# Optimization experiments

Measured on AMD Instinct MI355X. Metric: run time of the kernel, lower is better.

Reference implementation:

```python
import jax, jax.numpy as jnp
import numpy as np
from functools import partial

SAMPLE_RATE = 48000
BITRATE = 128000
M = 1024            # AAC_FRAME_LENGTH (hop, MDCT bins)
N = 2048            # AAC_WINDOW_LENGTH
TARGET_BITS = BITRATE * M / SAMPLE_RATE   # bits per frame (all channels)
MAX_GAIN = 120.0
EPS = 1e-9


def _window():
    # sine window satisfies Princen-Bradley: w[n]^2 + w[n+M]^2 = 1
    n = jnp.arange(N, dtype=jnp.float32)
    return jnp.sin(jnp.pi / N * (n + 0.5))


def _cosmat():
    # MDCT basis  C[n,k] = cos(pi/M (n + 0.5 + M/2)(k + 0.5)),  shape (N, M)
    n = jnp.arange(N, dtype=jnp.float32)[:, None]
    k = jnp.arange(M, dtype=jnp.float32)[None, :]
    return jnp.cos(jnp.pi / M * (n + 0.5 + M / 2) * (k + 0.5))


def _frame_bits(ax75, gain):
    """Estimated coded bits per frame under hard AAC power-law quantization.
    ax75: |coeff|^{3/4}, shape (B,F,C,M); gain: (B,F)."""
    inv = jnp.exp2(-0.75 * gain / 4.0)[:, :, None, None]
    qmag = jnp.round(ax75 * inv)
    # sign-magnitude style cost: nonzero -> floor(log2|q|)+2 bits, zero -> 1 bit
    bits = jnp.where(qmag > 0.0,
                     jnp.floor(jnp.log2(jnp.maximum(qmag, 1.0))) + 2.0,
                     1.0)
    return jnp.sum(bits, axis=(2, 3))  # (B,F)


def _find_global_gain(coeffs_bfcm):
    """Integer binary search for smallest gain with bits <= TARGET_BITS. (no grad)"""
    ax75 = jnp.abs(jax.lax.stop_gradient(coeffs_bfcm)) ** 0.75
    B, F = ax75.shape[0], ax75.shape[1]
    lo = jnp.zeros((B, F), jnp.float32)
    hi = jnp.full((B, F), MAX_GAIN, jnp.float32)

    def body(_, carry):
        lo, hi = carry
        mid = jnp.floor((lo + hi) / 2.0)
        too_big = _frame_bits(ax75, mid) > TARGET_BITS
        lo = jnp.where(too_big, mid + 1.0, lo)
        hi = jnp.where(too_big, hi, mid)
        return lo, hi

    _, hi = jax.lax.fori_loop(0, 8, body, (lo, hi))  # 8 iters covers [0,120]
    return hi  # (B,F)


def reference(audio):
    B, C, T = audio.shape
    w = _window()
    Cm = _cosmat()

    # --- frame_audio: left-pad M, right-pad to full frames ---
    F = -(-(T + M) // M)
    pad_right = F * M + M - (T + M)
    x = jnp.pad(audio, ((0, 0), (0, 0), (M, pad_right)))
    idx = jnp.arange(F)[:, None] * M + jnp.arange(N)[None, :]      # (F,N)
    frames = x[:, :, idx]                                          # (B,C,F,N)

    # --- analysis window + MDCT ---
    windowed = frames * w
    coeffs = jnp.einsum('bcfn,nk->bcfk', windowed, Cm)             # (B,C,F,M)
    coeffs_bfcm = jnp.transpose(coeffs, (0, 2, 1, 3))              # (B,F,C,M)

    # --- iterative global-gain search (hard quant, no grad) ---
    gains = _find_global_gain(coeffs_bfcm)                         # (B,F)

    # --- quantize (STE) / dequantize: q = round((|x| 2^{-g/4})^{3/4}) ---
    scale = jnp.exp2(gains / 4.0)[:, :, None, None]
    sgn = jnp.sign(coeffs_bfcm)
    q_soft = sgn * (jnp.abs(coeffs_bfcm) / scale + EPS) ** 0.75
    q = q_soft + jax.lax.stop_gradient(jnp.round(q_soft) - q_soft)
    dq = jnp.sign(q) * jnp.abs(q) ** (4.0 / 3.0) * scale           # (B,F,C,M)

    # --- IMDCT + synthesis window ---
    dq_bcfm = jnp.transpose(dq, (0, 2, 1, 3))                      # (B,C,F,M)
    td = (2.0 / M) * jnp.einsum('bcfk,nk->bcfn', dq_bcfm, Cm)      # (B,C,F,N)
    rew = td * w

    # --- overlap-add (hop M) ---
    out = jnp.zeros((B, C, (F + 1) * M), audio.dtype)
    out = out.at[:, :, :F * M].add(rew[:, :, :, :M].reshape(B, C, F * M))
    out = out.at[:, :, M:].add(rew[:, :, :, M:].reshape(B, C, F * M))
    return out[:, :, M:M + T]


def setup_inputs() -> dict:
    key = jax.random.key(0)
    audio = 0.5 * jax.random.normal(key, (8, 2, 1440000), dtype=jnp.float32)
    return {"audio": audio}
```

## Files before the change

kernel.cpp:

```cpp
#include <hip/hip_runtime.h>
#include <math.h>

#define B_ 8
#define C_ 2
#define T_ 1440000
#define F_ 1408
#define R_ 22528
#define TARGET_HI 2731

#define OFF_CFH 0ull
#define OFF_CFL (4ull << 20)
#define OFF_CIH (8ull << 20)
#define OFF_WF  (12ull << 20)
#define OFF_CF  (13ull << 20)
#define OFF_DQ  (OFF_CF + (size_t)R_ * 1024 * 4)

typedef _Float16 f16x8 __attribute__((ext_vector_type(8)));
typedef _Float16 f16x4 __attribute__((ext_vector_type(4)));
typedef float f32x16 __attribute__((ext_vector_type(16)));

__device__ inline f32x16 mfma16(f16x8 a, f16x8 b, f32x16 c) {
  return __builtin_amdgcn_mfma_f32_32x32x16_f16(a, b, c, 0, 0, 0);
}

__device__ inline void gld_lds16(const void* g, void* l) {
  __builtin_amdgcn_global_load_lds(
      (const __attribute__((address_space(1))) void*)g,
      (__attribute__((address_space(3))) void*)l, 16, 0, 0);
}

__global__ __launch_bounds__(256) void init_tables(char* wsb) {
  _Float16* cfh = (_Float16*)(wsb + OFF_CFH);
  _Float16* cfl = (_Float16*)(wsb + OFF_CFL);
  _Float16* cih = (_Float16*)(wsb + OFF_CIH);
  float*    wf  = (float*)(wsb + OFF_WF);
  int idx = blockIdx.x * 256 + threadIdx.x;
  if (idx < 2097152) {
    int n = idx >> 10, k = idx & 1023;
    const float c0 = (float)(M_PI / 1024.0);
    float a  = (float)n + 0.5f + 512.0f;
    float t1 = c0 * a;
    float ph = t1 * ((float)k + 0.5f);
    float cm = (float)cos((double)ph);
    _Float16 h = (_Float16)cm;
    _Float16 l = (_Float16)(cm - (float)h);
    cfh[(size_t)k * 2048 + n] = h;
    cfl[(size_t)k * 2048 + n] = l;
    cih[(size_t)n * 1024 + k] = h;
  } else if (idx < 2097152 + 2048) {
    int n = idx - 2097152;
    const float c1 = (float)(M_PI / 2048.0);
    float ph = c1 * ((float)n + 0.5f);
    wf[n] = (float)sin((double)ph);
  }
}

__global__ __launch_bounds__(256) void fwd_mfma(const float* __restrict__ audio,
                                                const char* __restrict__ wsb,
                                                float* __restrict__ coeffs) {
  __shared__ _Float16 Ah[128][40];
  __shared__ _Float16 Al[128][40];
  __shared__ _Float16 Bh[128][40];
  __shared__ _Float16 Bl[128][40];
  const _Float16* cfh = (const _Float16*)(wsb + OFF_CFH);
  const _Float16* cfl = (const _Float16*)(wsb + OFF_CFL);
  const float*    wf  = (const float*)(wsb + OFF_WF);

  int tid = threadIdx.x;
  int lane = tid & 63, wid = tid >> 6;
  int l31 = lane & 31, lHalf = lane >> 5;
  int waveM = wid >> 1, waveN = wid & 1;
  int rowTile = blockIdx.x * 128, colTile = blockIdx.y * 128;

  int sRow = tid >> 1;
  int sSeg = (tid & 1) << 4;
  int r = rowTile + sRow, bc = r / F_, f = r - bc * F_;
  const float* __restrict__ aud = audio + (size_t)bc * T_;
  int tBase = (f << 10) - 1024 + sSeg;
  const _Float16* bhp = cfh + (size_t)(colTile + sRow) * 2048 + sSeg;
  const _Float16* blp = cfl + (size_t)(colTile + sRow) * 2048 + sSeg;

  f32x16 acc[2][2];
#pragma unroll
  for (int i = 0; i < 2; i++)
#pragma unroll
    for (int j = 0; j < 2; j++)
#pragma unroll
      for (int e = 0; e < 16; e++) acc[i][j][e] = 0.f;

  for (int kt = 0; kt < 2048; kt += 32) {
    float av[16];
    int t0 = tBase + kt;
    if (t0 >= 0 && t0 + 16 <= T_) {
#pragma unroll
      for (int q = 0; q < 4; q++) {
        float4 x = *(const float4*)(aud + t0 + q * 4);
        av[q * 4 + 0] = x.x; av[q * 4 + 1] = x.y;
        av[q * 4 + 2] = x.z; av[q * 4 + 3] = x.w;
      }
    } else {
#pragma unroll
      for (int i = 0; i < 16; i++) {
        int t = t0 + i;
        av[i] = (t >= 0 && t < T_) ? aud[t] : 0.f;
      }
    }
    f16x8 vh[2], vl[2];
#pragma unroll
    for (int i = 0; i < 16; i++) {
      float v = av[i] * wf[kt + sSeg + i];
      _Float16 h = (_Float16)v;
      vh[i >> 3][i & 7] = h;
      vl[i >> 3][i & 7] = (_Float16)(v - (float)h);
    }
    float4 tb0 = *(const float4*)(bhp + kt);
    float4 tb1 = *(const float4*)(bhp + kt + 8);
    float4 tl0 = *(const float4*)(blp + kt);
    float4 tl1 = *(const float4*)(blp + kt + 8);

    __syncthreads();
    *(f16x8*)&Ah[sRow][sSeg]     = vh[0];
    *(f16x8*)&Ah[sRow][sSeg + 8] = vh[1];
    *(f16x8*)&Al[sRow][sSeg]     = vl[0];
    *(f16x8*)&Al[sRow][sSeg + 8] = vl[1];
    *(float4*)&Bh[sRow][sSeg]     = tb0;
    *(float4*)&Bh[sRow][sSeg + 8] = tb1;
    *(float4*)&Bl[sRow][sSeg]     = tl0;
    *(float4*)&Bl[sRow][sSeg + 8] = tl1;
    __syncthreads();

#pragma unroll
    for (int kc = 0; kc < 2; kc++) {
      int ko = kc * 16 + lHalf * 8;
      f16x8 a_h[2], a_l[2], b_h[2], b_l[2];
#pragma unroll
      for (int mi = 0; mi < 2; mi++) {
        a_h[mi] = *(const f16x8*)&Ah[waveM * 64 + mi * 32 + l31][ko];
        a_l[mi] = *(const f16x8*)&Al[waveM * 64 + mi * 32 + l31][ko];
      }
#pragma unroll
      for (int ni = 0; ni < 2; ni++) {
        b_h[ni] = *(const f16x8*)&Bh[waveN * 64 + ni * 32 + l31][ko];
        b_l[ni] = *(const f16x8*)&Bl[waveN * 64 + ni * 32 + l31][ko];
      }
#pragma unroll
      for (int mi = 0; mi < 2; mi++)
#pragma unroll
        for (int ni = 0; ni < 2; ni++) {
          acc[mi][ni] = mfma16(a_h[mi], b_h[ni], acc[mi][ni]);
          acc[mi][ni] = mfma16(a_h[mi], b_l[ni], acc[mi][ni]);
          acc[mi][ni] = mfma16(a_l[mi], b_h[ni], acc[mi][ni]);
        }
    }
  }

#pragma unroll
  for (int mi = 0; mi < 2; mi++)
#pragma unroll
    for (int ni = 0; ni < 2; ni++) {
      int col = colTile + waveN * 64 + ni * 32 + l31;
#pragma unroll
      for (int reg = 0; reg < 16; reg++) {
        int rowIn = (reg & 3) + 8 * (reg >> 2) + 4 * lHalf;
        int rr = rowTile + waveM * 64 + mi * 32 + rowIn;
        coeffs[(size_t)rr * 1024 + col] = acc[mi][ni][reg];
      }
    }
}

__global__ __launch_bounds__(256) void quantize(const float* __restrict__ cf,
                                                _Float16* __restrict__ dqh) {
  int wid = threadIdx.x >> 6, lane = threadIdx.x & 63;
  int bf = blockIdx.x * 4 + wid;
  int b = bf / F_, f = bf - b * F_;
  size_t base0 = ((size_t)(b * C_ + 0) * F_ + f) * 1024;
  size_t base1 = ((size_t)(b * C_ + 1) * F_ + f) * 1024;

  float x[32], ax75[32];
#pragma unroll
  for (int c = 0; c < 2; c++) {
    size_t bb = c ? base1 : base0;
#pragma unroll
    for (int j = 0; j < 4; j++) {
      float4 v = *(const float4*)(cf + bb + j * 256 + lane * 4);
      int o = c * 16 + j * 4;
      x[o + 0] = v.x; x[o + 1] = v.y; x[o + 2] = v.z; x[o + 3] = v.w;
    }
  }
#pragma unroll
  for (int u = 0; u < 32; u++) {
    float ax = fabsf(x[u]);
    float s  = sqrtf(ax);
    ax75[u]  = s * sqrtf(s);
  }

  int lo = 0, hi = 120;
#pragma unroll
  for (int it = 0; it < 8; it++) {
    int mid = (lo + hi) >> 1;
    float inv = exp2f(-0.1875f * (float)mid);
    int s = 0;
#pragma unroll
    for (int u = 0; u < 32; u++) {
      float qm = rintf(ax75[u] * inv);
      int iq = (int)qm;
      s += (iq > 0) ? (33 - __clz(iq)) : 1;
    }
#pragma unroll
    for (int off = 1; off < 64; off <<= 1) s += __shfl_xor(s, off, 64);
    if (s >= TARGET_HI) lo = mid + 1; else hi = mid;
  }

  float scale = exp2f(0.25f * (float)hi);
  float rs    = exp2f(-0.25f * (float)hi);
#pragma unroll
  for (int c = 0; c < 2; c++) {
    size_t bb = c ? base1 : base0;
#pragma unroll
    for (int j = 0; j < 4; j++) {
      f16x4 o4;
#pragma unroll
      for (int e = 0; e < 4; e++) {
        int u = c * 16 + j * 4 + e;
        float ax  = fabsf(x[u]);
        float t   = ax * rs + 1e-9f;
        float s1  = sqrtf(t);
        float qs  = s1 * sqrtf(s1);
        float q   = rintf(qs);
        float q43 = q * exp2f(__log2f(q) * (1.0f / 3.0f));
        o4[e] = (_Float16)copysignf(q43 * scale, x[u]);
      }
      *(f16x4*)(dqh + bb + j * 256 + lane * 4) = o4;
    }
  }
}

__global__ __launch_bounds__(256) void inv_gemm(const char* __restrict__ wsb,
                                                _Float16* __restrict__ tdh) {
  __shared__ __align__(16) _Float16 Ad[2][128][32];
  __shared__ __align__(16) _Float16 Bd[2][256][32];
  const _Float16* dqh = (const _Float16*)(wsb + OFF_DQ);
  const _Float16* cih = (const _Float16*)(wsb + OFF_CIH);
  const float*    wf  = (const float*)(wsb + OFF_WF);

  int tid = threadIdx.x;
  int lane = tid & 63, wid = tid >> 6;
  int l31 = lane & 31, lHalf = lane >> 5;
  int waveM = wid >> 1, waveN = wid & 1;
  int rowTile = blockIdx.x * 128, colTile = blockIdx.y * 256;

  int srcRow = lane >> 2;
  int swz = ((lane & 3) ^ ((lane >> 3) & 3)) << 3;
  const _Float16* aS = dqh + (size_t)(rowTile + wid * 32 + srcRow) * 1024 + swz;
  const _Float16* bS = cih + (size_t)(colTile + wid * 64 + srcRow) * 1024 + swz;

  auto stage = [&](int kt, int buf) {
    gld_lds16(aS + kt,             &Ad[buf][wid * 32][0]);
    gld_lds16(aS + kt + 16 * 1024, &Ad[buf][wid * 32 + 16][0]);
#pragma unroll
    for (int j = 0; j < 4; j++)
      gld_lds16(bS + kt + (size_t)j * 16 * 1024, &Bd[buf][wid * 64 + j * 16][0]);
  };

  f32x16 acc[2][4];
#pragma unroll
  for (int i = 0; i < 2; i++)
#pragma unroll
    for (int j = 0; j < 4; j++)
#pragma unroll
      for (int e = 0; e < 16; e++) acc[i][j][e] = 0.f;

  stage(0, 0);
  asm volatile("s_waitcnt vmcnt(0)" ::: "memory");
  __syncthreads();

  int cur = 0;
  for (int kt = 0; kt < 1024; kt += 32) {
    if (kt + 32 < 1024) stage(kt + 32, cur ^ 1);
#pragma unroll
    for (int kc = 0; kc < 2; kc++) {
      int slot = ((kc * 2 + lHalf) ^ ((l31 >> 1) & 3)) << 4;
      const char* ar = (const char*)&Ad[cur][waveM * 64 + l31][0];
      const char* br = (const char*)&Bd[cur][waveN * 128 + l31][0];
      f16x8 a0 = *(const f16x8*)(ar + slot);
      f16x8 a1 = *(const f16x8*)(ar + 32 * 64 + slot);
      f16x8 b0 = *(const f16x8*)(br + slot);
      f16x8 b1 = *(const f16x8*)(br + 32 * 64 + slot);
      f16x8 b2 = *(const f16x8*)(br + 64 * 64 + slot);
      f16x8 b3 = *(const f16x8*)(br + 96 * 64 + slot);
      acc[0][0] = mfma16(a0, b0, acc[0][0]);
      acc[0][1] = mfma16(a0, b1, acc[0][1]);
      acc[0][2] = mfma16(a0, b2, acc[0][2]);
      acc[0][3] = mfma16(a0, b3, acc[0][3]);
      acc[1][0] = mfma16(a1, b0, acc[1][0]);
      acc[1][1] = mfma16(a1, b1, acc[1][1]);
      acc[1][2] = mfma16(a1, b2, acc[1][2]);
      acc[1][3] = mfma16(a1, b3, acc[1][3]);
    }
    asm volatile("s_waitcnt vmcnt(0)" ::: "memory");
    __syncthreads();
    cur ^= 1;
  }

  const float sc = 2.0f / 1024.0f;
#pragma unroll
  for (int mi = 0; mi < 2; mi++)
#pragma unroll
    for (int ni = 0; ni < 4; ni++) {
      int n = colTile + waveN * 128 + ni * 32 + l31;
      float wv = wf[n] * sc;
#pragma unroll
      for (int reg = 0; reg < 16; reg++) {
        int rowIn = (reg & 3) + 8 * (reg >> 2) + 4 * lHalf;
        int rr = rowTile + waveM * 64 + mi * 32 + rowIn;
        tdh[(size_t)rr * 2048 + n] = (_Float16)(acc[mi][ni][reg] * wv);
      }
    }
}

__global__ __launch_bounds__(256) void ola(const char* __restrict__ wsb,
                                           float* __restrict__ out) {
  const _Float16* tdh = (const _Float16*)(wsb + OFF_CF);
  int idx = blockIdx.x * 256 + threadIdx.x;
  size_t base = (size_t)idx * 8;
  int bc = (int)(base / T_);
  int t  = (int)(base - (size_t)bc * T_);
  int g = t >> 10, o = t & 1023;
  size_t r0 = (size_t)bc * F_ + g;
  f16x8 hi = *(const f16x8*)(tdh + (r0 + 1) * 2048 + o);
  f16x8 lo = *(const f16x8*)(tdh + r0 * 2048 + 1024 + o);
  float4 v0, v1;
  v0.x = (float)hi[0] + (float)lo[0];
  v0.y = (float)hi[1] + (float)lo[1];
  v0.z = (float)hi[2] + (float)lo[2];
  v0.w = (float)hi[3] + (float)lo[3];
  v1.x = (float)hi[4] + (float)lo[4];
  v1.y = (float)hi[5] + (float)lo[5];
  v1.z = (float)hi[6] + (float)lo[6];
  v1.w = (float)hi[7] + (float)lo[7];
  *(float4*)(out + base)     = v0;
  *(float4*)(out + base + 4) = v1;
}

extern "C" void kernel_launch(void* const* d_in, const int* in_sizes, int n_in,
                              void* d_out, int out_size, void* d_ws, size_t ws_size,
                              hipStream_t stream) {
  const float* audio = (const float*)d_in[0];
  float* out = (float*)d_out;
  char* wsb  = (char*)d_ws;
  float*    cf  = (float*)(wsb + OFF_CF);
  _Float16* dqh = (_Float16*)(wsb + OFF_DQ);
  _Float16* tdh = (_Float16*)(wsb + OFF_CF);

  init_tables<<<(2097152 + 2048 + 255) / 256, 256, 0, stream>>>(wsb);
  fwd_mfma<<<dim3(R_ / 128, 1024 / 128), 256, 0, stream>>>(audio, wsb, cf);
  quantize<<<(B_ * F_) / 4, 256, 0, stream>>>(cf, dqh);
  inv_gemm<<<dim3(R_ / 128, 2048 / 256), 256, 0, stream>>>(wsb, tdh);
  ola<<<(B_ * C_ * T_) / (256 * 8), 256, 0, stream>>>(wsb, out);
}
```

Before: 798.1 us.

## Exploit IMDCT output symmetry to halve inverse GEMM columns

Because the IMDCT output has even/odd symmetry, only 1024 unique time samples per frame are computed (rows 0-511 and 1024-1535 of the basis), which halves the inverse GEMM's N dimension and its output writes. The synthesis window and the mirrored, sign-flipped reconstruction move into the overlap-add kernel, which now reads reversed segments and applies the window there. This relies on the mirror identities being exact in the indexing, and the reversed f16 reads add some index work to the OLA.

Measured after the change: 695.7 us. -12.8%, faster.

```diff
diff --git a/kernel.cpp b/kernel.cpp
--- a/kernel.cpp
+++ b/kernel.cpp
@@ -32,7 +32,7 @@
 __global__ __launch_bounds__(256) void init_tables(char* wsb) {
   _Float16* cfh = (_Float16*)(wsb + OFF_CFH);
   _Float16* cfl = (_Float16*)(wsb + OFF_CFL);
-  _Float16* cih = (_Float16*)(wsb + OFF_CIH);
+  _Float16* cif = (_Float16*)(wsb + OFF_CIH);
   float*    wf  = (float*)(wsb + OFF_WF);
   int idx = blockIdx.x * 256 + threadIdx.x;
   if (idx < 2097152) {
@@ -46,7 +46,8 @@
     _Float16 l = (_Float16)(cm - (float)h);
     cfh[(size_t)k * 2048 + n] = h;
     cfl[(size_t)k * 2048 + n] = l;
-    cih[(size_t)n * 1024 + k] = h;
+    if (n < 512)                    cif[(size_t)n * 1024 + k] = h;
+    else if (n >= 1024 && n < 1536) cif[(size_t)(n - 512) * 1024 + k] = h;
   } else if (idx < 2097152 + 2048) {
     int n = idx - 2097152;
     const float c1 = (float)(M_PI / 2048.0);
@@ -240,8 +241,7 @@
   __shared__ __align__(16) _Float16 Ad[2][128][32];
   __shared__ __align__(16) _Float16 Bd[2][256][32];
   const _Float16* dqh = (const _Float16*)(wsb + OFF_DQ);
-  const _Float16* cih = (const _Float16*)(wsb + OFF_CIH);
-  const float*    wf  = (const float*)(wsb + OFF_WF);
+  const _Float16* cif = (const _Float16*)(wsb + OFF_CIH);
 
   int tid = threadIdx.x;
   int lane = tid & 63, wid = tid >> 6;
@@ -252,7 +252,7 @@
   int srcRow = lane >> 2;
   int swz = ((lane & 3) ^ ((lane >> 3) & 3)) << 3;
   const _Float16* aS = dqh + (size_t)(rowTile + wid * 32 + srcRow) * 1024 + swz;
-  const _Float16* bS = cih + (size_t)(colTile + wid * 64 + srcRow) * 1024 + swz;
+  const _Float16* bS = cif + (size_t)(colTile + wid * 64 + srcRow) * 1024 + swz;
 
   auto stage = [&](int kt, int buf) {
     gld_lds16(aS + kt,             &Ad[buf][wid * 32][0]);
@@ -308,36 +308,48 @@
 #pragma unroll
     for (int ni = 0; ni < 4; ni++) {
       int n = colTile + waveN * 128 + ni * 32 + l31;
-      float wv = wf[n] * sc;
 #pragma unroll
       for (int reg = 0; reg < 16; reg++) {
         int rowIn = (reg & 3) + 8 * (reg >> 2) + 4 * lHalf;
         int rr = rowTile + waveM * 64 + mi * 32 + rowIn;
-        tdh[(size_t)rr * 2048 + n] = (_Float16)(acc[mi][ni][reg] * wv);
+        tdh[(size_t)rr * 1024 + n] = (_Float16)(acc[mi][ni][reg] * sc);
       }
     }
 }
 
 __global__ __launch_bounds__(256) void ola(const char* __restrict__ wsb,
                                            float* __restrict__ out) {
-  const _Float16* tdh = (const _Float16*)(wsb + OFF_CF);
+  const _Float16* tdu = (const _Float16*)(wsb + OFF_CF);
+  const float*    wf  = (const float*)(wsb + OFF_WF);
   int idx = blockIdx.x * 256 + threadIdx.x;
   size_t base = (size_t)idx * 8;
   int bc = (int)(base / T_);
   int t  = (int)(base - (size_t)bc * T_);
   int g = t >> 10, o = t & 1023;
   size_t r0 = (size_t)bc * F_ + g;
-  f16x8 hi = *(const f16x8*)(tdh + (r0 + 1) * 2048 + o);
-  f16x8 lo = *(const f16x8*)(tdh + r0 * 2048 + 1024 + o);
+  float w1[8], w2[8];
+  *(float4*)&w1[0] = *(const float4*)(wf + o);
+  *(float4*)&w1[4] = *(const float4*)(wf + o + 4);
+  *(float4*)&w2[0] = *(const float4*)(wf + 1024 + o);
+  *(float4*)&w2[4] = *(const float4*)(wf + 1024 + o + 4);
+  const float sc = 1.0f;
+  float rv[8];
+  if (o < 512) {
+    f16x8 a = *(const f16x8*)(tdu + (r0 + 1) * 1024 + o);
+    f16x8 b = *(const f16x8*)(tdu + r0 * 1024 + 512 + o);
+#pragma unroll
+    for (int i = 0; i < 8; i++)
+      rv[i] = (w1[i] * (float)a[i] + w2[i] * (float)b[i]) * sc;
+  } else {
+    f16x8 a = *(const f16x8*)(tdu + (r0 + 1) * 1024 + (1016 - o));
+    f16x8 b = *(const f16x8*)(tdu + r0 * 1024 + (1528 - o));
+#pragma unroll
+    for (int i = 0; i < 8; i++)
+      rv[i] = (w2[i] * (float)b[7 - i] - w1[i] * (float)a[7 - i]) * sc;
+  }
   float4 v0, v1;
-  v0.x = (float)hi[0] + (float)lo[0];
-  v0.y = (float)hi[1] + (float)lo[1];
-  v0.z = (float)hi[2] + (float)lo[2];
-  v0.w = (float)hi[3] + (float)lo[3];
-  v1.x = (float)hi[4] + (float)lo[4];
-  v1.y = (float)hi[5] + (float)lo[5];
-  v1.z = (float)hi[6] + (float)lo[6];
-  v1.w = (float)hi[7] + (float)lo[7];
+  v0.x = rv[0]; v0.y = rv[1]; v0.z = rv[2]; v0.w = rv[3];
+  v1.x = rv[4]; v1.y = rv[5]; v1.z = rv[6]; v1.w = rv[7];
   *(float4*)(out + base)     = v0;
   *(float4*)(out + base + 4) = v1;
 }
@@ -355,6 +367,6 @@
   init_tables<<<(2097152 + 2048 + 255) / 256, 256, 0, stream>>>(wsb);
   fwd_mfma<<<dim3(R_ / 128, 1024 / 128), 256, 0, stream>>>(audio, wsb, cf);
   quantize<<<(B_ * F_) / 4, 256, 0, stream>>>(cf, dqh);
-  inv_gemm<<<dim3(R_ / 128, 2048 / 256), 256, 0, stream>>>(wsb, tdh);
+  inv_gemm<<<dim3(R_ / 128, 1024 / 256), 256, 0, stream>>>(wsb, tdh);
   ola<<<(B_ * C_ * T_) / (256 * 8), 256, 0, stream>>>(wsb, out);
 }
```
